# Kernel optimization log

Hardware: AMD Instinct MI355X
Metric: run time of the kernel (lower is better)

The kernel has to match this reference:

```python
import jax, jax.numpy as jnp
import numpy as np

B, S, D = 2, 2048, 2048
H = 32
HD = D // H  # 64


def setup_inputs() -> dict:
    key = jax.random.key(0)
    ks = jax.random.split(key, 7)
    s = 1.0 / np.sqrt(D)
    return {
        "hidden_states": jax.random.normal(ks[0], (B, S, D), dtype=jnp.float32),
        "Wq": jax.random.normal(ks[1], (D, D), dtype=jnp.float32) * s,
        "Wk": jax.random.normal(ks[2], (D, D), dtype=jnp.float32) * s,
        "Wv": jax.random.normal(ks[3], (D, D), dtype=jnp.float32) * s,
        "Wf": jax.random.normal(ks[4], (H, D), dtype=jnp.float32) * s,
        "bf": jax.random.normal(ks[5], (H,), dtype=jnp.float32) * 0.1,
        "Wo": jax.random.normal(ks[6], (D, D), dtype=jnp.float32) * s,
    }


def _forgetting_attn(x, Wq, Wk, Wv, Wf, bf, Wo):
    b, s, _ = x.shape
    # projections (torch Linear: y = x @ W.T)
    q = (x @ Wq.T).reshape(b, s, H, HD)
    k = (x @ Wk.T).reshape(b, s, H, HD)
    v = (x @ Wv.T).reshape(b, s, H, HD)
    # per-head log-sigmoid forget gates, fp32, cumulative sum over time
    f = jax.nn.log_sigmoid((x @ Wf.T + bf).astype(jnp.float32))  # [b, s, H]
    c = jnp.cumsum(f, axis=1)  # [b, s, H]
    scale = 1.0 / np.sqrt(HD)
    # scores with forget bias: c_i - c_j
    scores = jnp.einsum("bihd,bjhd->bhij", q, k) * scale
    scores = scores + (c[:, :, None, :] - c[:, None, :, :]).transpose(0, 3, 1, 2)
    causal = jnp.tril(jnp.ones((s, s), dtype=bool))
    scores = jnp.where(causal[None, None], scores, -jnp.inf)
    p = jax.nn.softmax(scores, axis=-1)
    o = jnp.einsum("bhij,bjhd->bihd", p, v).reshape(b, s, D)
    return o @ Wo.T


def reference(hidden_states, Wq, Wk, Wv, Wf, bf, Wo):
    return _forgetting_attn(hidden_states, Wq, Wk, Wv, Wf, bf, Wo)
```

## Files before the change

### kernel.cpp

```cpp
#include <hip/hip_runtime.h>
#include <math.h>

#define B 2
#define S 2048
#define D 2048
#define H 32
#define HD 64
#define M (B*S)

typedef short s16x8 __attribute__((ext_vector_type(8)));
typedef float f32x4 __attribute__((ext_vector_type(4)));

__device__ __forceinline__ unsigned short f2bf(float f) {
    unsigned u = __float_as_uint(f);
    return (unsigned short)((u + 0x7fffu + ((u >> 16) & 1u)) >> 16);
}
__device__ __forceinline__ float bf2f(unsigned short h) {
    return __uint_as_float(((unsigned)h) << 16);
}

#define GBM 128
#define GBN 128
#define GBK 32
#define GLD (GBK + 8)

__global__ __launch_bounds__(256) void gemm_bf16x3(
    const float* __restrict__ A, const float* __restrict__ Bw,
    float* __restrict__ Cm, int Ndim, int Kdim)
{
    __shared__ unsigned short Ah[GBM * GLD], Al[GBM * GLD];
    __shared__ unsigned short Bh[GBN * GLD], Bl[GBN * GLD];
    const int tid = threadIdx.x;
    const int nwg = gridDim.x, cpx = nwg >> 3;
    const int wg = (blockIdx.x & 7) * cpx + (blockIdx.x >> 3);
    const int ntn = Ndim / GBN;
    const int m0 = (wg / ntn) * GBM, n0 = (wg % ntn) * GBN;

    const int row = tid >> 1;
    const int seg = (tid & 1) << 4;
    const float* Arow = A + (size_t)(m0 + row) * Kdim + seg;
    const float* Brow = Bw + (size_t)(n0 + row) * Kdim + seg;
    const int sbase = row * GLD + seg;

    const int wv = tid >> 6, lane = tid & 63;
    const int wr = (wv >> 1) << 6, wc = (wv & 1) << 6;
    const int fr = lane & 15, ko = (lane >> 4) << 3;

    f32x4 acc[4][4] = {};
    for (int k0 = 0; k0 < Kdim; k0 += GBK) {
        {
            float fa[16], fb[16];
            #pragma unroll
            for (int j4 = 0; j4 < 4; ++j4) {
                *(float4*)&fa[j4 * 4] = *(const float4*)(Arow + k0 + j4 * 4);
                *(float4*)&fb[j4 * 4] = *(const float4*)(Brow + k0 + j4 * 4);
            }
            unsigned short hv[16], lv[16], hw[16], lw[16];
            #pragma unroll
            for (int j = 0; j < 16; ++j) {
                unsigned short h = f2bf(fa[j]);
                hv[j] = h; lv[j] = f2bf(fa[j] - bf2f(h));
                unsigned short g = f2bf(fb[j]);
                hw[j] = g; lw[j] = f2bf(fb[j] - bf2f(g));
            }
            *(s16x8*)&Ah[sbase]     = *(s16x8*)&hv[0];
            *(s16x8*)&Ah[sbase + 8] = *(s16x8*)&hv[8];
            *(s16x8*)&Al[sbase]     = *(s16x8*)&lv[0];
            *(s16x8*)&Al[sbase + 8] = *(s16x8*)&lv[8];
            *(s16x8*)&Bh[sbase]     = *(s16x8*)&hw[0];
            *(s16x8*)&Bh[sbase + 8] = *(s16x8*)&hw[8];
            *(s16x8*)&Bl[sbase]     = *(s16x8*)&lw[0];
            *(s16x8*)&Bl[sbase + 8] = *(s16x8*)&lw[8];
        }
        __syncthreads();
        s16x8 fah[4], fal[4], fbh[4], fbl[4];
        #pragma unroll
        for (int m = 0; m < 4; ++m) {
            const int r = (wr + m * 16 + fr) * GLD + ko;
            fah[m] = *(s16x8*)&Ah[r];
            fal[m] = *(s16x8*)&Al[r];
        }
        #pragma unroll
        for (int n = 0; n < 4; ++n) {
            const int r = (wc + n * 16 + fr) * GLD + ko;
            fbh[n] = *(s16x8*)&Bh[r];
            fbl[n] = *(s16x8*)&Bl[r];
        }
        #pragma unroll
        for (int m = 0; m < 4; ++m)
            #pragma unroll
            for (int n = 0; n < 4; ++n) {
                acc[m][n] = __builtin_amdgcn_mfma_f32_16x16x32_bf16(fah[m], fbh[n], acc[m][n], 0, 0, 0);
                acc[m][n] = __builtin_amdgcn_mfma_f32_16x16x32_bf16(fah[m], fbl[n], acc[m][n], 0, 0, 0);
                acc[m][n] = __builtin_amdgcn_mfma_f32_16x16x32_bf16(fal[m], fbh[n], acc[m][n], 0, 0, 0);
            }
        __syncthreads();
    }
    const int crow0 = m0 + wr + ((lane >> 4) << 2);
    const int ccol0 = n0 + wc + fr;
    #pragma unroll
    for (int m = 0; m < 4; ++m)
        #pragma unroll
        for (int n = 0; n < 4; ++n)
            #pragma unroll
            for (int r = 0; r < 4; ++r)
                Cm[(size_t)(crow0 + m * 16 + r) * Ndim + ccol0 + n * 16] = acc[m][n][r];
}

__global__ __launch_bounds__(256) void fgate_kernel(
    const float* __restrict__ x, const float* __restrict__ Wf,
    const float* __restrict__ bfv, float* __restrict__ F)
{
    __shared__ float xs[D];
    const int bs = blockIdx.x;
    const float* xr = x + (size_t)bs * D;
    for (int i = threadIdx.x * 4; i < D; i += 256 * 4)
        *(float4*)&xs[i] = *(const float4*)&xr[i];
    __syncthreads();
    const int wave = threadIdx.x >> 6, lane = threadIdx.x & 63;
    for (int h = wave * 8; h < wave * 8 + 8; ++h) {
        const float* wr = Wf + (size_t)h * D;
        float sum = 0.f;
        for (int i = lane * 4; i < D; i += 64 * 4) {
            float4 w4 = *(const float4*)&wr[i];
            sum += xs[i]*w4.x + xs[i+1]*w4.y + xs[i+2]*w4.z + xs[i+3]*w4.w;
        }
        #pragma unroll
        for (int off = 32; off > 0; off >>= 1) sum += __shfl_down(sum, off);
        if (lane == 0) {
            float z = sum + bfv[h];
            F[(size_t)bs * H + h] = fminf(z, 0.f) - log1pf(expf(-fabsf(z)));
        }
    }
}

__global__ __launch_bounds__(256) void cumsum_kernel(float* __restrict__ F)
{
    const int b = blockIdx.x >> 5;
    const int h = blockIdx.x & 31;
    float* base = F + (size_t)b * S * H + h;
    __shared__ float part[256];
    const int t = threadIdx.x;
    float v[8];
    float run = 0.f;
    #pragma unroll
    for (int i = 0; i < 8; ++i) {
        v[i] = base[(size_t)(t * 8 + i) * H];
        run += v[i];
        v[i] = run;
    }
    part[t] = run;
    __syncthreads();
    for (int off = 1; off < 256; off <<= 1) {
        float add = (t >= off) ? part[t - off] : 0.f;
        __syncthreads();
        part[t] += add;
        __syncthreads();
    }
    const float offs = (t > 0) ? part[t - 1] : 0.f;
    #pragma unroll
    for (int i = 0; i < 8; ++i)
        base[(size_t)(t * 8 + i) * H] = v[i] + offs;
}

#define QBLK 128
#define KV 64
#define PLD 72
#define SCALE 0.125f

__global__ __launch_bounds__(256, 2) void attn_mfma(
    const float* __restrict__ Q, const float* __restrict__ Km,
    const float* __restrict__ V, const float* __restrict__ C,
    float* __restrict__ O)
{
    __shared__ unsigned short Qh[QBLK * PLD], Ql[QBLK * PLD];
    __shared__ unsigned short Ks[KV * PLD];
    __shared__ unsigned short Vt[HD * PLD];
    __shared__ unsigned short Pb[4 * 32 * PLD];
    __shared__ float cj[KV];

    const int qt = (int)gridDim.x - 1 - blockIdx.x;
    const int b = blockIdx.z >> 5, h = blockIdx.z & 31;
    const int q0 = qt * QBLK;
    const int tid = threadIdx.x, wv = tid >> 6, lane = tid & 63;
    const int g = lane >> 4, fr = lane & 15;

    {
        const int row = tid >> 1;
        const int seg = (tid & 1) << 5;
        const float* src = Q + (size_t)(b * S + q0 + row) * D + h * HD + seg;
        float f[32];
        #pragma unroll
        for (int j4 = 0; j4 < 8; ++j4)
            *(float4*)&f[j4 * 4] = *(const float4*)(src + j4 * 4);
        unsigned short hv[32], lv[32];
        #pragma unroll
        for (int e = 0; e < 32; ++e) {
            unsigned short hh = f2bf(f[e]);
            hv[e] = hh; lv[e] = f2bf(f[e] - bf2f(hh));
        }
        const int sb = row * PLD + seg;
        #pragma unroll
        for (int e = 0; e < 4; ++e) {
            *(s16x8*)&Qh[sb + e * 8] = *(s16x8*)&hv[e * 8];
            *(s16x8*)&Ql[sb + e * 8] = *(s16x8*)&lv[e * 8];
        }
    }
    __syncthreads();

    s16x8 qfh[2][2], qfl[2][2];
    #pragma unroll
    for (int m = 0; m < 2; ++m)
        #pragma unroll
        for (int kd = 0; kd < 2; ++kd) {
            const int r = (wv * 32 + m * 16 + fr) * PLD + kd * 32 + g * 8;
            qfh[m][kd] = *(s16x8*)&Qh[r];
            qfl[m][kd] = *(s16x8*)&Ql[r];
        }

    f32x4 Oa[2][4] = {};
    float mr[2][4], lr[2][4];
    #pragma unroll
    for (int m = 0; m < 2; ++m)
        #pragma unroll
        for (int r = 0; r < 4; ++r) { mr[m][r] = -INFINITY; lr[m][r] = 0.f; }

    const int imax = q0 + wv * 32 + 31;
    const int nj = (q0 + QBLK) / KV;
    unsigned short* Pw = &Pb[wv * 32 * PLD];

    for (int jt = 0; jt < nj; ++jt) {
        const int j0 = jt * KV;
        {
            const int row = tid >> 2;
            const int seg = (tid & 3) << 4;
            const size_t goff = (size_t)(b * S + j0 + row) * D + h * HD + seg;
            float kf[16], vf[16];
            #pragma unroll
            for (int j4 = 0; j4 < 4; ++j4) {
                *(float4*)&kf[j4 * 4] = *(const float4*)(Km + goff + j4 * 4);
                *(float4*)&vf[j4 * 4] = *(const float4*)(V + goff + j4 * 4);
            }
            unsigned short kb[16];
            #pragma unroll
            for (int e = 0; e < 16; ++e) kb[e] = f2bf(kf[e]);
            *(s16x8*)&Ks[row * PLD + seg]     = *(s16x8*)&kb[0];
            *(s16x8*)&Ks[row * PLD + seg + 8] = *(s16x8*)&kb[8];
            #pragma unroll
            for (int e = 0; e < 16; ++e)
                Vt[(seg + e) * PLD + row] = f2bf(vf[e]);
            if (tid < KV)
                cj[tid] = C[(size_t)(b * S + j0 + tid) * H + h];
        }
        __syncthreads();

        if (j0 <= imax) {
            s16x8 kfr[4][2];
            #pragma unroll
            for (int n = 0; n < 4; ++n)
                #pragma unroll
                for (int kd = 0; kd < 2; ++kd)
                    kfr[n][kd] = *(s16x8*)&Ks[(n * 16 + fr) * PLD + kd * 32 + g * 8];
            f32x4 sa[2][4] = {};
            #pragma unroll
            for (int m = 0; m < 2; ++m)
                #pragma unroll
                for (int n = 0; n < 4; ++n) {
                    #pragma unroll
                    for (int kd = 0; kd < 2; ++kd) {
                        sa[m][n] = __builtin_amdgcn_mfma_f32_16x16x32_bf16(qfh[m][kd], kfr[n][kd], sa[m][n], 0, 0, 0);
                        sa[m][n] = __builtin_amdgcn_mfma_f32_16x16x32_bf16(qfl[m][kd], kfr[n][kd], sa[m][n], 0, 0, 0);
                    }
                }
            float cjr[4];
            #pragma unroll
            for (int n = 0; n < 4; ++n) cjr[n] = cj[fr + 16 * n];
            float sc[2][4][4];
            float tm[2][4];
            #pragma unroll
            for (int m = 0; m < 2; ++m)
                #pragma unroll
                for (int r = 0; r < 4; ++r) tm[m][r] = -INFINITY;
            #pragma unroll
            for (int m = 0; m < 2; ++m)
                #pragma unroll
                for (int n = 0; n < 4; ++n)
                    #pragma unroll
                    for (int r = 0; r < 4; ++r) {
                        const int qrow = q0 + wv * 32 + m * 16 + g * 4 + r;
                        const int jcol = j0 + fr + 16 * n;
                        float s = sa[m][n][r] * SCALE - cjr[n];
                        s = (jcol <= qrow) ? s : -INFINITY;
                        sc[m][n][r] = s;
                        tm[m][r] = fmaxf(tm[m][r], s);
                    }
            #pragma unroll
            for (int m = 0; m < 2; ++m)
                #pragma unroll
                for (int r = 0; r < 4; ++r) {
                    float v = tm[m][r];
                    v = fmaxf(v, __shfl_xor(v, 1));
                    v = fmaxf(v, __shfl_xor(v, 2));
                    v = fmaxf(v, __shfl_xor(v, 4));
                    v = fmaxf(v, __shfl_xor(v, 8));
                    tm[m][r] = v;
                }
            #pragma unroll
            for (int m = 0; m < 2; ++m)
                #pragma unroll
                for (int r = 0; r < 4; ++r) {
                    const float newm = fmaxf(mr[m][r], tm[m][r]);
                    const float corr = __expf(mr[m][r] - newm);
                    mr[m][r] = newm;
                    lr[m][r] *= corr;
                    #pragma unroll
                    for (int n = 0; n < 4; ++n) Oa[m][n][r] *= corr;
                }
            #pragma unroll
            for (int m = 0; m < 2; ++m) {
                float ps[4];
                #pragma unroll
                for (int r = 0; r < 4; ++r) ps[r] = 0.f;
                #pragma unroll
                for (int n = 0; n < 4; ++n)
                    #pragma unroll
                    for (int r = 0; r < 4; ++r) {
                        const float p = __expf(sc[m][n][r] - mr[m][r]);
                        ps[r] += p;
                        Pw[(m * 16 + g * 4 + r) * PLD + fr + 16 * n] = f2bf(p);
                    }
                #pragma unroll
                for (int r = 0; r < 4; ++r) {
                    float v = ps[r];
                    v += __shfl_xor(v, 1);
                    v += __shfl_xor(v, 2);
                    v += __shfl_xor(v, 4);
                    v += __shfl_xor(v, 8);
                    lr[m][r] += v;
                }
            }
            s16x8 pf[2][2], vfr[4][2];
            #pragma unroll
            for (int m = 0; m < 2; ++m)
                #pragma unroll
                for (int kj = 0; kj < 2; ++kj)
                    pf[m][kj] = *(s16x8*)&Pw[(fr + 16 * m) * PLD + kj * 32 + g * 8];
            #pragma unroll
            for (int n = 0; n < 4; ++n)
                #pragma unroll
                for (int kj = 0; kj < 2; ++kj)
                    vfr[n][kj] = *(s16x8*)&Vt[(n * 16 + fr) * PLD + kj * 32 + g * 8];
            #pragma unroll
            for (int m = 0; m < 2; ++m)
                #pragma unroll
                for (int n = 0; n < 4; ++n)
                    #pragma unroll
                    for (int kj = 0; kj < 2; ++kj)
                        Oa[m][n] = __builtin_amdgcn_mfma_f32_16x16x32_bf16(pf[m][kj], vfr[n][kj], Oa[m][n], 0, 0, 0);
        }
        __syncthreads();
    }

    #pragma unroll
    for (int m = 0; m < 2; ++m)
        #pragma unroll
        for (int r = 0; r < 4; ++r) {
            const float inv = 1.f / lr[m][r];
            const size_t row = (size_t)(b * S + q0 + wv * 32 + m * 16 + g * 4 + r);
            #pragma unroll
            for (int n = 0; n < 4; ++n)
                O[row * D + h * HD + fr + 16 * n] = Oa[m][n][r] * inv;
        }
}

extern "C" void kernel_launch(void* const* d_in, const int* in_sizes, int n_in,
                              void* d_out, int out_size, void* d_ws, size_t ws_size,
                              hipStream_t stream) {
    const float* x  = (const float*)d_in[0];
    const float* Wq = (const float*)d_in[1];
    const float* Wk = (const float*)d_in[2];
    const float* Wv = (const float*)d_in[3];
    const float* Wf = (const float*)d_in[4];
    const float* bf = (const float*)d_in[5];
    const float* Wo = (const float*)d_in[6];
    float* out = (float*)d_out;

    float* Q  = (float*)d_ws;
    float* K  = Q + (size_t)M * D;
    float* V  = K + (size_t)M * D;
    float* Fc = V + (size_t)M * D;
    float* O  = Fc + (size_t)M * H;

    const dim3 gblk(256);
    const dim3 ggrid((M / GBM) * (D / GBN));
    gemm_bf16x3<<<ggrid, gblk, 0, stream>>>(x, Wq, Q, D, D);
    gemm_bf16x3<<<ggrid, gblk, 0, stream>>>(x, Wk, K, D, D);
    gemm_bf16x3<<<ggrid, gblk, 0, stream>>>(x, Wv, V, D, D);
    fgate_kernel<<<dim3(M), gblk, 0, stream>>>(x, Wf, bf, Fc);
    cumsum_kernel<<<dim3(B * H), gblk, 0, stream>>>(Fc);
    attn_mfma<<<dim3(S / QBLK, 1, B * H), gblk, 0, stream>>>(Q, K, V, Fc, O);
    gemm_bf16x3<<<ggrid, gblk, 0, stream>>>(O, Wo, out, D, D);
}
```

Baseline: 977.8 us.

## Pre-split operands into bf16 hi/lo buffers and pass bf16 between stages

Adds a split kernel that converts x and each weight into bf16 hi/lo arrays once. The GEMMs then load pre-split bf16 tiles instead of converting fp32 inside every tile, and they emit bf16 Q(hi/lo), K and V directly. The attention kernel reads bf16 Q fragments straight from global memory, drops the Q shared buffers, raises occupancy to 4 blocks, and writes O as hi/lo bf16 for the final GEMM. The aim is to cut redundant conversion work and halve global traffic between stages. The cost is extra split-kernel launches plus a workspace buffer that is reused for both X and O.

New measurement: 982.3 us. Within noise of the previous version (+0.5%).

```diff
diff --git a/kernel.cpp b/kernel.cpp
--- a/kernel.cpp
+++ b/kernel.cpp
@@ -19,14 +19,35 @@
     return __uint_as_float(((unsigned)h) << 16);
 }
 
+__global__ __launch_bounds__(256) void split_kernel(
+    const float* __restrict__ in, unsigned short* __restrict__ hi,
+    unsigned short* __restrict__ lo, int n)
+{
+    const int idx = (blockIdx.x * 256 + threadIdx.x) * 8;
+    if (idx >= n) return;
+    float f[8];
+    *(float4*)&f[0] = *(const float4*)(in + idx);
+    *(float4*)&f[4] = *(const float4*)(in + idx + 4);
+    unsigned short h[8], l[8];
+    #pragma unroll
+    for (int e = 0; e < 8; ++e) {
+        h[e] = f2bf(f[e]);
+        l[e] = f2bf(f[e] - bf2f(h[e]));
+    }
+    *(s16x8*)&hi[idx] = *(s16x8*)&h[0];
+    *(s16x8*)&lo[idx] = *(s16x8*)&l[0];
+}
+
 #define GBM 128
 #define GBN 128
 #define GBK 32
 #define GLD (GBK + 8)
 
-__global__ __launch_bounds__(256) void gemm_bf16x3(
-    const float* __restrict__ A, const float* __restrict__ Bw,
-    float* __restrict__ Cm, int Ndim, int Kdim)
+__global__ __launch_bounds__(256) void gemm_pre(
+    const unsigned short* __restrict__ Agh, const unsigned short* __restrict__ Agl,
+    const unsigned short* __restrict__ Bgh, const unsigned short* __restrict__ Bgl,
+    float* __restrict__ Cf, unsigned short* __restrict__ Ch,
+    unsigned short* __restrict__ Cl, int Ndim, int Kdim)
 {
     __shared__ unsigned short Ah[GBM * GLD], Al[GBM * GLD];
     __shared__ unsigned short Bh[GBN * GLD], Bl[GBN * GLD];
@@ -38,8 +59,8 @@
 
     const int row = tid >> 1;
     const int seg = (tid & 1) << 4;
-    const float* Arow = A + (size_t)(m0 + row) * Kdim + seg;
-    const float* Brow = Bw + (size_t)(n0 + row) * Kdim + seg;
+    const size_t abase = (size_t)(m0 + row) * Kdim + seg;
+    const size_t bbase = (size_t)(n0 + row) * Kdim + seg;
     const int sbase = row * GLD + seg;
 
     const int wv = tid >> 6, lane = tid & 63;
@@ -48,30 +69,14 @@
 
     f32x4 acc[4][4] = {};
     for (int k0 = 0; k0 < Kdim; k0 += GBK) {
-        {
-            float fa[16], fb[16];
-            #pragma unroll
-            for (int j4 = 0; j4 < 4; ++j4) {
-                *(float4*)&fa[j4 * 4] = *(const float4*)(Arow + k0 + j4 * 4);
-                *(float4*)&fb[j4 * 4] = *(const float4*)(Brow + k0 + j4 * 4);
-            }
-            unsigned short hv[16], lv[16], hw[16], lw[16];
-            #pragma unroll
-            for (int j = 0; j < 16; ++j) {
-                unsigned short h = f2bf(fa[j]);
-                hv[j] = h; lv[j] = f2bf(fa[j] - bf2f(h));
-                unsigned short g = f2bf(fb[j]);
-                hw[j] = g; lw[j] = f2bf(fb[j] - bf2f(g));
-            }
-            *(s16x8*)&Ah[sbase]     = *(s16x8*)&hv[0];
-            *(s16x8*)&Ah[sbase + 8] = *(s16x8*)&hv[8];
-            *(s16x8*)&Al[sbase]     = *(s16x8*)&lv[0];
-            *(s16x8*)&Al[sbase + 8] = *(s16x8*)&lv[8];
-            *(s16x8*)&Bh[sbase]     = *(s16x8*)&hw[0];
-            *(s16x8*)&Bh[sbase + 8] = *(s16x8*)&hw[8];
-            *(s16x8*)&Bl[sbase]     = *(s16x8*)&lw[0];
-            *(s16x8*)&Bl[sbase + 8] = *(s16x8*)&lw[8];
-        }
+        *(s16x8*)&Ah[sbase]     = *(const s16x8*)&Agh[abase + k0];
+        *(s16x8*)&Ah[sbase + 8] = *(const s16x8*)&Agh[abase + k0 + 8];
+        *(s16x8*)&Al[sbase]     = *(const s16x8*)&Agl[abase + k0];
+        *(s16x8*)&Al[sbase + 8] = *(const s16x8*)&Agl[abase + k0 + 8];
+        *(s16x8*)&Bh[sbase]     = *(const s16x8*)&Bgh[bbase + k0];
+        *(s16x8*)&Bh[sbase + 8] = *(const s16x8*)&Bgh[bbase + k0 + 8];
+        *(s16x8*)&Bl[sbase]     = *(const s16x8*)&Bgl[bbase + k0];
+        *(s16x8*)&Bl[sbase + 8] = *(const s16x8*)&Bgl[bbase + k0 + 8];
         __syncthreads();
         s16x8 fah[4], fal[4], fbh[4], fbl[4];
         #pragma unroll
@@ -103,8 +108,16 @@
         #pragma unroll
         for (int n = 0; n < 4; ++n)
             #pragma unroll
-            for (int r = 0; r < 4; ++r)
-                Cm[(size_t)(crow0 + m * 16 + r) * Ndim + ccol0 + n * 16] = acc[m][n][r];
+            for (int r = 0; r < 4; ++r) {
+                const float c = acc[m][n][r];
+                const size_t idx = (size_t)(crow0 + m * 16 + r) * Ndim + ccol0 + n * 16;
+                if (Cf) Cf[idx] = c;
+                if (Ch) {
+                    const unsigned short hh = f2bf(c);
+                    Ch[idx] = hh;
+                    if (Cl) Cl[idx] = f2bf(c - bf2f(hh));
+                }
+            }
 }
 
 __global__ __launch_bounds__(256) void fgate_kernel(
@@ -168,12 +181,12 @@
 #define PLD 72
 #define SCALE 0.125f
 
-__global__ __launch_bounds__(256, 2) void attn_mfma(
-    const float* __restrict__ Q, const float* __restrict__ Km,
-    const float* __restrict__ V, const float* __restrict__ C,
-    float* __restrict__ O)
+__global__ __launch_bounds__(256, 4) void attn_mfma2(
+    const unsigned short* __restrict__ Qh, const unsigned short* __restrict__ Ql,
+    const unsigned short* __restrict__ Kh, const unsigned short* __restrict__ Vh,
+    const float* __restrict__ C,
+    unsigned short* __restrict__ Oh, unsigned short* __restrict__ Ol)
 {
-    __shared__ unsigned short Qh[QBLK * PLD], Ql[QBLK * PLD];
     __shared__ unsigned short Ks[KV * PLD];
     __shared__ unsigned short Vt[HD * PLD];
     __shared__ unsigned short Pb[4 * 32 * PLD];
@@ -185,38 +198,18 @@
     const int tid = threadIdx.x, wv = tid >> 6, lane = tid & 63;
     const int g = lane >> 4, fr = lane & 15;
 
+    s16x8 qfh[2][2], qfl[2][2];
     {
-        const int row = tid >> 1;
-        const int seg = (tid & 1) << 5;
-        const float* src = Q + (size_t)(b * S + q0 + row) * D + h * HD + seg;
-        float f[32];
-        #pragma unroll
-        for (int j4 = 0; j4 < 8; ++j4)
-            *(float4*)&f[j4 * 4] = *(const float4*)(src + j4 * 4);
-        unsigned short hv[32], lv[32];
-        #pragma unroll
-        for (int e = 0; e < 32; ++e) {
-            unsigned short hh = f2bf(f[e]);
-            hv[e] = hh; lv[e] = f2bf(f[e] - bf2f(hh));
-        }
-        const int sb = row * PLD + seg;
-        #pragma unroll
-        for (int e = 0; e < 4; ++e) {
-            *(s16x8*)&Qh[sb + e * 8] = *(s16x8*)&hv[e * 8];
-            *(s16x8*)&Ql[sb + e * 8] = *(s16x8*)&lv[e * 8];
-        }
-    }
-    __syncthreads();
-
-    s16x8 qfh[2][2], qfl[2][2];
-    #pragma unroll
-    for (int m = 0; m < 2; ++m)
-        #pragma unroll
-        for (int kd = 0; kd < 2; ++kd) {
-            const int r = (wv * 32 + m * 16 + fr) * PLD + kd * 32 + g * 8;
-            qfh[m][kd] = *(s16x8*)&Qh[r];
-            qfl[m][kd] = *(s16x8*)&Ql[r];
-        }
+        const size_t qb = (size_t)(b * S + q0 + wv * 32) * D + h * HD;
+        #pragma unroll
+        for (int m = 0; m < 2; ++m)
+            #pragma unroll
+            for (int kd = 0; kd < 2; ++kd) {
+                const size_t off = qb + (size_t)(m * 16 + fr) * D + kd * 32 + g * 8;
+                qfh[m][kd] = *(const s16x8*)&Qh[off];
+                qfl[m][kd] = *(const s16x8*)&Ql[off];
+            }
+    }
 
     f32x4 Oa[2][4] = {};
     float mr[2][4], lr[2][4];
@@ -235,20 +228,15 @@
             const int row = tid >> 2;
             const int seg = (tid & 3) << 4;
             const size_t goff = (size_t)(b * S + j0 + row) * D + h * HD + seg;
-            float kf[16], vf[16];
-            #pragma unroll
-            for (int j4 = 0; j4 < 4; ++j4) {
-                *(float4*)&kf[j4 * 4] = *(const float4*)(Km + goff + j4 * 4);
-                *(float4*)&vf[j4 * 4] = *(const float4*)(V + goff + j4 * 4);
-            }
-            unsigned short kb[16];
-            #pragma unroll
-            for (int e = 0; e < 16; ++e) kb[e] = f2bf(kf[e]);
-            *(s16x8*)&Ks[row * PLD + seg]     = *(s16x8*)&kb[0];
-            *(s16x8*)&Ks[row * PLD + seg + 8] = *(s16x8*)&kb[8];
-            #pragma unroll
-            for (int e = 0; e < 16; ++e)
-                Vt[(seg + e) * PLD + row] = f2bf(vf[e]);
+            *(s16x8*)&Ks[row * PLD + seg]     = *(const s16x8*)&Kh[goff];
+            *(s16x8*)&Ks[row * PLD + seg + 8] = *(const s16x8*)&Kh[goff + 8];
+            s16x8 v0 = *(const s16x8*)&Vh[goff];
+            s16x8 v1 = *(const s16x8*)&Vh[goff + 8];
+            #pragma unroll
+            for (int e = 0; e < 8; ++e) {
+                Vt[(seg + e) * PLD + row]     = (unsigned short)v0[e];
+                Vt[(seg + 8 + e) * PLD + row] = (unsigned short)v1[e];
+            }
             if (tid < KV)
                 cj[tid] = C[(size_t)(b * S + j0 + tid) * H + h];
         }
@@ -366,10 +354,14 @@
         #pragma unroll
         for (int r = 0; r < 4; ++r) {
             const float inv = 1.f / lr[m][r];
-            const size_t row = (size_t)(b * S + q0 + wv * 32 + m * 16 + g * 4 + r);
-            #pragma unroll
-            for (int n = 0; n < 4; ++n)
-                O[row * D + h * HD + fr + 16 * n] = Oa[m][n][r] * inv;
+            const size_t rowb = (size_t)(b * S + q0 + wv * 32 + m * 16 + g * 4 + r) * D + h * HD;
+            #pragma unroll
+            for (int n = 0; n < 4; ++n) {
+                const float c = Oa[m][n][r] * inv;
+                const unsigned short hh = f2bf(c);
+                Oh[rowb + fr + 16 * n] = hh;
+                Ol[rowb + fr + 16 * n] = f2bf(c - bf2f(hh));
+            }
         }
 }
 
@@ -385,19 +377,34 @@
     const float* Wo = (const float*)d_in[6];
     float* out = (float*)d_out;
 
-    float* Q  = (float*)d_ws;
-    float* K  = Q + (size_t)M * D;
-    float* V  = K + (size_t)M * D;
-    float* Fc = V + (size_t)M * D;
-    float* O  = Fc + (size_t)M * H;
-
-    const dim3 gblk(256);
+    const size_t MD = (size_t)M * D, DD = (size_t)D * D;
+    unsigned short* Xh = (unsigned short*)d_ws;
+    unsigned short* Xl = Xh + MD;
+    unsigned short* Wh = Xl + MD;
+    unsigned short* Wl = Wh + DD;
+    unsigned short* Qh = Wl + DD;
+    unsigned short* Ql = Qh + MD;
+    unsigned short* Kh = Ql + MD;
+    unsigned short* Vh = Kh + MD;
+    float* Fc = (float*)(Vh + MD);
+    unsigned short* Oh = Xh;
+    unsigned short* Ol = Xl;
+
+    const dim3 blk(256);
     const dim3 ggrid((M / GBM) * (D / GBN));
-    gemm_bf16x3<<<ggrid, gblk, 0, stream>>>(x, Wq, Q, D, D);
-    gemm_bf16x3<<<ggrid, gblk, 0, stream>>>(x, Wk, K, D, D);
-    gemm_bf16x3<<<ggrid, gblk, 0, stream>>>(x, Wv, V, D, D);
-    fgate_kernel<<<dim3(M), gblk, 0, stream>>>(x, Wf, bf, Fc);
-    cumsum_kernel<<<dim3(B * H), gblk, 0, stream>>>(Fc);
-    attn_mfma<<<dim3(S / QBLK, 1, B * H), gblk, 0, stream>>>(Q, K, V, Fc, O);
-    gemm_bf16x3<<<ggrid, gblk, 0, stream>>>(O, Wo, out, D, D);
-}
+    const int nMD = (int)MD, nDD = (int)DD;
+    const dim3 gsx(nMD / 8 / 256), gsw(nDD / 8 / 256);
+
+    split_kernel<<<gsx, blk, 0, stream>>>(x, Xh, Xl, nMD);
+    split_kernel<<<gsw, blk, 0, stream>>>(Wq, Wh, Wl, nDD);
+    gemm_pre<<<ggrid, blk, 0, stream>>>(Xh, Xl, Wh, Wl, nullptr, Qh, Ql, D, D);
+    split_kernel<<<gsw, blk, 0, stream>>>(Wk, Wh, Wl, nDD);
+    gemm_pre<<<ggrid, blk, 0, stream>>>(Xh, Xl, Wh, Wl, nullptr, Kh, nullptr, D, D);
+    split_kernel<<<gsw, blk, 0, stream>>>(Wv, Wh, Wl, nDD);
+    gemm_pre<<<ggrid, blk, 0, stream>>>(Xh, Xl, Wh, Wl, nullptr, Vh, nullptr, D, D);
+    fgate_kernel<<<dim3(M), blk, 0, stream>>>(x, Wf, bf, Fc);
+    cumsum_kernel<<<dim3(B * H), blk, 0, stream>>>(Fc);
+    attn_mfma2<<<dim3(S / QBLK, 1, B * H), blk, 0, stream>>>(Qh, Ql, Kh, Vh, Fc, Oh, Ol);
+    split_kernel<<<gsw, blk, 0, stream>>>(Wo, Wh, Wl, nDD);
+    gemm_pre<<<ggrid, blk, 0, stream>>>(Oh, Ol, Wh, Wl, out, nullptr, nullptr, D, D);
+}
```
